# Kernel optimization log

Measured on AMD Instinct MI355X. Metric: run time of the kernel, lower is better.

The kernel has to match this reference:

```python
import jax, jax.numpy as jnp
import numpy as np

D_MODEL = 2048
SSM_RANK = 4            # ultimate_config.ar_ssm_max_rank
FFN_RANK = max(D_MODEL // 128, 2)  # = 16
EPS = 1e-6


def rmsnorm(x, w):
    # shared RMSNorm: x * w / rms(x)
    ms = jnp.mean(jnp.square(x), axis=-1, keepdims=True)
    return x * jax.lax.rsqrt(ms + EPS) * w


def ar_ssm(x, V, U, a_logit):
    # low-rank (rank r) semiseparable SSM:
    #   u_t = V^T x_t            [B,S,r]
    #   h_t = a * h_{t-1} + u_t  (per-rank learned decay a in (0,1))
    #   y_t = U h_t              [B,S,D]
    a = jax.nn.sigmoid(a_logit)               # [r]
    u = jnp.einsum('bsd,dr->bsr', x, V)       # [B,S,r]
    u_t = jnp.swapaxes(u, 0, 1)               # [S,B,r]

    def step(h, u_s):
        h = a * h + u_s
        return h, h

    h0 = jnp.zeros(u_t.shape[1:], dtype=x.dtype)   # [B,r]
    h_last, hs = jax.lax.scan(step, h0, u_t)        # hs: [S,B,r]
    hs = jnp.swapaxes(hs, 0, 1)                     # [B,S,r]
    y = jnp.einsum('bsr,dr->bsd', hs, U)
    return y, h_last


def ffn(x, W1, W2):
    return jnp.einsum('bsr,rd->bsd', jax.nn.gelu(jnp.einsum('bsd,dr->bsr', x, W1)), W2)


def setup_inputs() -> dict:
    key = jax.random.key(0)
    ks = jax.random.split(key, 7)
    B, S, D, R, RF = 4, 4096, D_MODEL, SSM_RANK, FFN_RANK
    x = jax.random.normal(ks[0], (B, S, D), dtype=jnp.float32)
    norm_w = jnp.ones((D,), dtype=jnp.float32)
    V = jax.random.normal(ks[1], (D, R), dtype=jnp.float32) / np.sqrt(D)
    U = jax.random.normal(ks[2], (D, R), dtype=jnp.float32) / np.sqrt(R)
    a_logit = jax.random.normal(ks[3], (R,), dtype=jnp.float32)
    W1 = jax.random.normal(ks[4], (D, RF), dtype=jnp.float32) / np.sqrt(D)
    W2 = jax.random.normal(ks[5], (RF, D), dtype=jnp.float32) / np.sqrt(RF)
    return {"x": x, "norm_w": norm_w, "V": V, "U": U, "a_logit": a_logit, "W1": W1, "W2": W2}


def reference(x, norm_w, V, U, a_logit, W1, W2):
    x_ar, _ = ar_ssm(rmsnorm(x, norm_w), V, U, a_logit)
    x = x + x_ar
    x = x + ffn(rmsnorm(x, norm_w), W1, W2)
    return x
```

## Files before the change

kernel.cpp:

```cpp
#include <hip/hip_runtime.h>
#include <math.h>
#include <stdint.h>

#define D 2048
#define S_LEN 4096
#define NB 4
#define NTOK (NB * S_LEN)

__device__ __forceinline__ float gelu_tanh(float v) {
    const float c = 0.7978845608028654f;
    float t = tanhf(c * (v + 0.044715f * v * v * v));
    return 0.5f * v * (1.0f + t);
}

__device__ __forceinline__ void gload_lds16(const float* g, float* l) {
    __builtin_amdgcn_global_load_lds(
        (const __attribute__((address_space(1))) void*)g,
        (__attribute__((address_space(3))) void*)(uintptr_t)(uint32_t)(uintptr_t)l,
        16, 0, 0);
}

__global__ __launch_bounds__(256) void k0_transpose(
        const float* __restrict__ W1, const float* __restrict__ V, const float* __restrict__ U,
        float* __restrict__ W1t, float* __restrict__ Vt, float* __restrict__ Ut)
{
    const int id = blockIdx.x * 256 + threadIdx.x;
    if (id < D * 16) {
        const int d = id >> 4, f = id & 15;
        W1t[f * D + d] = W1[id];
    } else if (id < D * 16 + D * 4) {
        const int i2 = id - D * 16;
        Vt[(i2 & 3) * D + (i2 >> 2)] = V[i2];
    } else {
        const int i2 = id - D * 16 - D * 4;
        Ut[(i2 & 3) * D + (i2 >> 2)] = U[i2];
    }
}

__global__ __launch_bounds__(256, 4) void k1_u_kernel(
        const float* __restrict__ x, const float* __restrict__ nw,
        const float* __restrict__ Vt, float* __restrict__ u)
{
    const int gwave = (blockIdx.x * 256 + threadIdx.x) >> 6;
    const int lane  = threadIdx.x & 63;
    const int t0 = gwave * 2;

    float ss[2] = {0.f, 0.f};
    float uv[2][4] = {};

    #pragma unroll
    for (int j = 0; j < 8; ++j) {
        const int d0 = j * 256 + lane * 4;
        const float4 nw4 = *reinterpret_cast<const float4*>(nw + d0);
        float4 z4[2];
        #pragma unroll
        for (int tk = 0; tk < 2; ++tk) {
            const float4 xv = *reinterpret_cast<const float4*>(x + (size_t)(t0 + tk) * D + d0);
            ss[tk] += xv.x*xv.x + xv.y*xv.y + xv.z*xv.z + xv.w*xv.w;
            z4[tk].x = xv.x*nw4.x; z4[tk].y = xv.y*nw4.y;
            z4[tk].z = xv.z*nw4.z; z4[tk].w = xv.w*nw4.w;
        }
        #pragma unroll
        for (int r = 0; r < 4; ++r) {
            const float4 vv = *reinterpret_cast<const float4*>(Vt + r * D + d0);
            #pragma unroll
            for (int tk = 0; tk < 2; ++tk)
                uv[tk][r] += z4[tk].x*vv.x + z4[tk].y*vv.y + z4[tk].z*vv.z + z4[tk].w*vv.w;
        }
    }
    #pragma unroll
    for (int m = 1; m < 64; m <<= 1) {
        #pragma unroll
        for (int tk = 0; tk < 2; ++tk) {
            ss[tk] += __shfl_xor(ss[tk], m);
            #pragma unroll
            for (int r = 0; r < 4; ++r) uv[tk][r] += __shfl_xor(uv[tk][r], m);
        }
    }
    if (lane < 8) {
        float ssv = ss[0], uvv = uv[0][0];
        #pragma unroll
        for (int tk = 0; tk < 2; ++tk)
            #pragma unroll
            for (int r = 0; r < 4; ++r)
                if (lane == tk * 4 + r) { ssv = ss[tk]; uvv = uv[tk][r]; }
        const float rstd = rsqrtf(ssv * (1.0f / 2048.0f) + 1e-6f);
        u[(size_t)t0 * 4 + lane] = rstd * uvv;
    }
}

__global__ __launch_bounds__(256) void k2_scan_kernel(
        const float* __restrict__ u, const float* __restrict__ a_logit,
        float* __restrict__ hs)
{
    __shared__ float lds[256];
    const int b = blockIdx.x >> 2;
    const int r = blockIdx.x & 3;
    const int i = threadIdx.x;
    const float a = 1.0f / (1.0f + expf(-a_logit[r]));
    const float* up = u  + (size_t)b * S_LEN * 4 + r;
    float*       hp = hs + (size_t)b * S_LEN * 4 + r;

    float ul[16];
    float h = 0.f;
    const int s0 = i * 16;
    #pragma unroll
    for (int k = 0; k < 16; ++k) { ul[k] = up[(size_t)(s0 + k) * 4]; h = a * h + ul[k]; }

    const float a2 = a*a, a4 = a2*a2, a8 = a4*a4;
    float m = a8 * a8;
    float run = h;
    lds[i] = run;
    for (int off = 1; off < 256; off <<= 1) {
        __syncthreads();
        const float v = (i >= off) ? lds[i - off] : 0.f;
        __syncthreads();
        run += m * v;
        lds[i] = run;
        m *= m;
    }
    __syncthreads();
    float hh = (i == 0) ? 0.f : lds[i - 1];
    #pragma unroll
    for (int k = 0; k < 16; ++k) { hh = a * hh + ul[k]; hp[(size_t)(s0 + k) * 4] = hh; }
}

#define SLICE_F 5376
__global__ __launch_bounds__(256) void k3_fused_kernel(
        const float* __restrict__ x, const float* __restrict__ nw,
        const float* __restrict__ Ut, const float* __restrict__ hs,
        const float* __restrict__ W1t, const float* __restrict__ W2,
        float* __restrict__ out)
{
    __shared__ float buf[2][SLICE_F];
    __shared__ float reds[4][2][20];
    __shared__ float tvs[4][32];
    const int w = threadIdx.x >> 6;
    const int lane = threadIdx.x & 63;
    const int t0 = (blockIdx.x * 4 + w) * 2;
    const float4* hs4 = reinterpret_cast<const float4*>(hs);
    float4 hv[2];
    #pragma unroll
    for (int tk = 0; tk < 2; ++tk) hv[tk] = hs4[t0 + tk];

    float ss[2] = {0.f, 0.f};
    float pf[2][16] = {};

    for (int s = w; s < 21; s += 4) {
        const float* src = (s == 0) ? (nw)
                         : (s < 5)  ? (Ut + (size_t)(s - 1) * D)
                                    : (W1t + (size_t)(s - 5) * D);
        gload_lds16(src + lane * 4, &buf[0][s * 256 + lane * 4]);
    }
    __syncthreads();

    for (int j = 0; j < 8; ++j) {
        const int cur = j & 1;
        if (j < 7) {
            const int jn = (j + 1) * 256;
            for (int s = w; s < 21; s += 4) {
                const float* src = (s == 0) ? (nw + jn)
                                 : (s < 5)  ? (Ut + (size_t)(s - 1) * D + jn)
                                            : (W1t + (size_t)(s - 5) * D + jn);
                gload_lds16(src + lane * 4, &buf[cur ^ 1][s * 256 + lane * 4]);
            }
        }
        const float* bw = buf[cur];
        const int d0 = j * 256 + lane * 4;
        const float4 nw4 = *reinterpret_cast<const float4*>(bw + lane * 4);
        float4 ut[4];
        #pragma unroll
        for (int r = 0; r < 4; ++r)
            ut[r] = *reinterpret_cast<const float4*>(bw + 256 + r * 256 + lane * 4);
        float4 z4[2];
        #pragma unroll
        for (int tk = 0; tk < 2; ++tk) {
            const float4 xv = *reinterpret_cast<const float4*>(x + (size_t)(t0 + tk) * D + d0);
            const float x20 = xv.x + hv[tk].x*ut[0].x + hv[tk].y*ut[1].x + hv[tk].z*ut[2].x + hv[tk].w*ut[3].x;
            const float x21 = xv.y + hv[tk].x*ut[0].y + hv[tk].y*ut[1].y + hv[tk].z*ut[2].y + hv[tk].w*ut[3].y;
            const float x22 = xv.z + hv[tk].x*ut[0].z + hv[tk].y*ut[1].z + hv[tk].z*ut[2].z + hv[tk].w*ut[3].z;
            const float x23 = xv.w + hv[tk].x*ut[0].w + hv[tk].y*ut[1].w + hv[tk].z*ut[2].w + hv[tk].w*ut[3].w;
            ss[tk] += x20*x20 + x21*x21 + x22*x22 + x23*x23;
            float4 x2v; x2v.x = x20; x2v.y = x21; x2v.z = x22; x2v.w = x23;
            *reinterpret_cast<float4*>(out + (size_t)(t0 + tk) * D + d0) = x2v;
            z4[tk].x = x20*nw4.x; z4[tk].y = x21*nw4.y;
            z4[tk].z = x22*nw4.z; z4[tk].w = x23*nw4.w;
        }
        #pragma unroll
        for (int f = 0; f < 16; ++f) {
            const float4 wv = *reinterpret_cast<const float4*>(bw + 1280 + f * 256 + lane * 4);
            #pragma unroll
            for (int tk = 0; tk < 2; ++tk)
                pf[tk][f] += z4[tk].x*wv.x + z4[tk].y*wv.y + z4[tk].z*wv.z + z4[tk].w*wv.w;
        }
        __syncthreads();
    }

    #pragma unroll
    for (int m = 1; m < 64; m <<= 1) {
        #pragma unroll
        for (int tk = 0; tk < 2; ++tk) {
            ss[tk] += __shfl_xor(ss[tk], m);
            #pragma unroll
            for (int f = 0; f < 16; ++f) pf[tk][f] += __shfl_xor(pf[tk][f], m);
        }
    }
    if (lane == 0) {
        #pragma unroll
        for (int tk = 0; tk < 2; ++tk) {
            reds[w][tk][16] = ss[tk];
            #pragma unroll
            for (int f = 0; f < 16; ++f) reds[w][tk][f] = pf[tk][f];
        }
    }
    __syncthreads();
    if (lane < 32) {
        const int mytk = lane >> 4, myf = lane & 15;
        const float rstd = rsqrtf(reds[w][mytk][16] * (1.0f / 2048.0f) + 1e-6f);
        tvs[w][lane] = gelu_tanh(rstd * reds[w][mytk][myf]);
    }
    __syncthreads();
    float tvv[2][16];
    #pragma unroll
    for (int tk = 0; tk < 2; ++tk)
        #pragma unroll
        for (int f = 0; f < 16; ++f) tvv[tk][f] = tvs[w][tk * 16 + f];

    for (int s = w; s < 16; s += 4)
        gload_lds16(W2 + (size_t)s * D + lane * 4, &buf[0][s * 256 + lane * 4]);
    __syncthreads();

    for (int j = 0; j < 8; ++j) {
        const int cur = j & 1;
        if (j < 7) {
            const int jn = (j + 1) * 256;
            for (int s = w; s < 16; s += 4)
                gload_lds16(W2 + (size_t)s * D + jn + lane * 4, &buf[cur ^ 1][s * 256 + lane * 4]);
        }
        const float* bw = buf[cur];
        const int d0 = j * 256 + lane * 4;
        float4 acc[2];
        #pragma unroll
        for (int tk = 0; tk < 2; ++tk)
            acc[tk] = *reinterpret_cast<const float4*>(out + (size_t)(t0 + tk) * D + d0);
        #pragma unroll
        for (int f = 0; f < 16; ++f) {
            const float4 w2v = *reinterpret_cast<const float4*>(bw + f * 256 + lane * 4);
            #pragma unroll
            for (int tk = 0; tk < 2; ++tk) {
                acc[tk].x += tvv[tk][f] * w2v.x;
                acc[tk].y += tvv[tk][f] * w2v.y;
                acc[tk].z += tvv[tk][f] * w2v.z;
                acc[tk].w += tvv[tk][f] * w2v.w;
            }
        }
        #pragma unroll
        for (int tk = 0; tk < 2; ++tk)
            *reinterpret_cast<float4*>(out + (size_t)(t0 + tk) * D + d0) = acc[tk];
        __syncthreads();
    }
}

extern "C" void kernel_launch(void* const* d_in, const int* in_sizes, int n_in,
                              void* d_out, int out_size, void* d_ws, size_t ws_size,
                              hipStream_t stream)
{
    (void)in_sizes; (void)n_in; (void)out_size; (void)ws_size;
    const float* x  = (const float*)d_in[0];
    const float* nw = (const float*)d_in[1];
    const float* V  = (const float*)d_in[2];
    const float* U  = (const float*)d_in[3];
    const float* al = (const float*)d_in[4];
    const float* W1 = (const float*)d_in[5];
    const float* W2 = (const float*)d_in[6];
    float* out = (float*)d_out;
    float* u   = (float*)d_ws;
    float* hs  = u + (size_t)NTOK * 4;
    float* W1t = hs + (size_t)NTOK * 4;
    float* Vt  = W1t + (size_t)16 * D;
    float* Ut  = Vt + (size_t)4 * D;

    k0_transpose  <<<dim3(192),       dim3(256), 0, stream>>>(W1, V, U, W1t, Vt, Ut);
    k1_u_kernel   <<<dim3(NTOK / 8),  dim3(256), 0, stream>>>(x, nw, Vt, u);
    k2_scan_kernel<<<dim3(16),        dim3(256), 0, stream>>>(u, al, hs);
    k3_fused_kernel<<<dim3(NTOK / 8), dim3(256), 0, stream>>>(x, nw, Ut, hs, W1t, W2, out);
}
```

Before: 339.0 us.

## Recompute residual in second pass, stage weights in LDS, vectorize scan over ranks

The fused kernel no longer writes the intermediate x+SSM residual to the output and reads it back. The second pass recomputes it from x, hs and U, with U staged in LDS next to W2, which removes one full-tensor write and read of output traffic. The u kernel now stages the norm weights and V in LDS once per block instead of reading them from global memory per wave. The scan uses one 1024-thread block per batch that handles all four ranks as float4, in place of 16 blocks each handling one rank with strided loads. This cuts scattered accesses, but the scan now runs on only four blocks.

```diff
diff --git a/kernel.cpp b/kernel.cpp
--- a/kernel.cpp
+++ b/kernel.cpp
@@ -37,13 +37,21 @@
     }
 }
 
-__global__ __launch_bounds__(256, 4) void k1_u_kernel(
+__global__ __launch_bounds__(256) void k1_u_kernel(
         const float* __restrict__ x, const float* __restrict__ nw,
         const float* __restrict__ Vt, float* __restrict__ u)
 {
-    const int gwave = (blockIdx.x * 256 + threadIdx.x) >> 6;
+    __shared__ float lw[10240];
+    const int w = threadIdx.x >> 6;
     const int lane  = threadIdx.x & 63;
-    const int t0 = gwave * 2;
+    const int t0 = ((blockIdx.x * 256 + threadIdx.x) >> 6) * 2;
+
+    for (int s = w; s < 40; s += 4) {
+        const int base = s * 256;
+        const float* src = (base < 2048) ? (nw + base) : (Vt + base - 2048);
+        gload_lds16(src + lane * 4, &lw[base + lane * 4]);
+    }
+    __syncthreads();
 
     float ss[2] = {0.f, 0.f};
     float uv[2][4] = {};
@@ -51,7 +59,7 @@
     #pragma unroll
     for (int j = 0; j < 8; ++j) {
         const int d0 = j * 256 + lane * 4;
-        const float4 nw4 = *reinterpret_cast<const float4*>(nw + d0);
+        const float4 nw4 = *reinterpret_cast<const float4*>(lw + d0);
         float4 z4[2];
         #pragma unroll
         for (int tk = 0; tk < 2; ++tk) {
@@ -62,7 +70,7 @@
         }
         #pragma unroll
         for (int r = 0; r < 4; ++r) {
-            const float4 vv = *reinterpret_cast<const float4*>(Vt + r * D + d0);
+            const float4 vv = *reinterpret_cast<const float4*>(lw + 2048 + r * 2048 + d0);
             #pragma unroll
             for (int tk = 0; tk < 2; ++tk)
                 uv[tk][r] += z4[tk].x*vv.x + z4[tk].y*vv.y + z4[tk].z*vv.z + z4[tk].w*vv.w;
@@ -89,40 +97,58 @@
     }
 }
 
-__global__ __launch_bounds__(256) void k2_scan_kernel(
+__global__ __launch_bounds__(1024) void k2_scan_kernel(
         const float* __restrict__ u, const float* __restrict__ a_logit,
         float* __restrict__ hs)
 {
-    __shared__ float lds[256];
-    const int b = blockIdx.x >> 2;
-    const int r = blockIdx.x & 3;
+    __shared__ float4 lds[1024];
+    const int b = blockIdx.x;
     const int i = threadIdx.x;
-    const float a = 1.0f / (1.0f + expf(-a_logit[r]));
-    const float* up = u  + (size_t)b * S_LEN * 4 + r;
-    float*       hp = hs + (size_t)b * S_LEN * 4 + r;
-
-    float ul[16];
-    float h = 0.f;
-    const int s0 = i * 16;
-    #pragma unroll
-    for (int k = 0; k < 16; ++k) { ul[k] = up[(size_t)(s0 + k) * 4]; h = a * h + ul[k]; }
-
-    const float a2 = a*a, a4 = a2*a2, a8 = a4*a4;
-    float m = a8 * a8;
-    float run = h;
+    const float4 al4 = *reinterpret_cast<const float4*>(a_logit);
+    float4 a;
+    a.x = 1.0f / (1.0f + expf(-al4.x));
+    a.y = 1.0f / (1.0f + expf(-al4.y));
+    a.z = 1.0f / (1.0f + expf(-al4.z));
+    a.w = 1.0f / (1.0f + expf(-al4.w));
+    const float4* up = reinterpret_cast<const float4*>(u) + (size_t)b * S_LEN;
+    float4*       hp = reinterpret_cast<float4*>(hs)      + (size_t)b * S_LEN;
+
+    const int s0 = i * 4;
+    float4 ul[4];
+    float4 h; h.x = 0.f; h.y = 0.f; h.z = 0.f; h.w = 0.f;
+    #pragma unroll
+    for (int k = 0; k < 4; ++k) {
+        ul[k] = up[s0 + k];
+        h.x = a.x * h.x + ul[k].x; h.y = a.y * h.y + ul[k].y;
+        h.z = a.z * h.z + ul[k].z; h.w = a.w * h.w + ul[k].w;
+    }
+
+    float4 m;
+    m.x = a.x*a.x; m.y = a.y*a.y; m.z = a.z*a.z; m.w = a.w*a.w;
+    m.x *= m.x; m.y *= m.y; m.z *= m.z; m.w *= m.w;
+    float4 run = h;
     lds[i] = run;
-    for (int off = 1; off < 256; off <<= 1) {
+    for (int off = 1; off < 1024; off <<= 1) {
         __syncthreads();
-        const float v = (i >= off) ? lds[i - off] : 0.f;
+        float4 v;
+        if (i >= off) v = lds[i - off];
+        else { v.x = 0.f; v.y = 0.f; v.z = 0.f; v.w = 0.f; }
         __syncthreads();
-        run += m * v;
+        run.x += m.x * v.x; run.y += m.y * v.y;
+        run.z += m.z * v.z; run.w += m.w * v.w;
         lds[i] = run;
-        m *= m;
-    }
-    __syncthreads();
-    float hh = (i == 0) ? 0.f : lds[i - 1];
-    #pragma unroll
-    for (int k = 0; k < 16; ++k) { hh = a * hh + ul[k]; hp[(size_t)(s0 + k) * 4] = hh; }
+        m.x *= m.x; m.y *= m.y; m.z *= m.z; m.w *= m.w;
+    }
+    __syncthreads();
+    float4 hh;
+    if (i == 0) { hh.x = 0.f; hh.y = 0.f; hh.z = 0.f; hh.w = 0.f; }
+    else hh = lds[i - 1];
+    #pragma unroll
+    for (int k = 0; k < 4; ++k) {
+        hh.x = a.x * hh.x + ul[k].x; hh.y = a.y * hh.y + ul[k].y;
+        hh.z = a.z * hh.z + ul[k].z; hh.w = a.w * hh.w + ul[k].w;
+        hp[s0 + k] = hh;
+    }
 }
 
 #define SLICE_F 5376
@@ -181,8 +207,6 @@
             const float x22 = xv.z + hv[tk].x*ut[0].z + hv[tk].y*ut[1].z + hv[tk].z*ut[2].z + hv[tk].w*ut[3].z;
             const float x23 = xv.w + hv[tk].x*ut[0].w + hv[tk].y*ut[1].w + hv[tk].z*ut[2].w + hv[tk].w*ut[3].w;
             ss[tk] += x20*x20 + x21*x21 + x22*x22 + x23*x23;
-            float4 x2v; x2v.x = x20; x2v.y = x21; x2v.z = x22; x2v.w = x23;
-            *reinterpret_cast<float4*>(out + (size_t)(t0 + tk) * D + d0) = x2v;
             z4[tk].x = x20*nw4.x; z4[tk].y = x21*nw4.y;
             z4[tk].z = x22*nw4.z; z4[tk].w = x23*nw4.w;
         }
@@ -226,26 +250,41 @@
         #pragma unroll
         for (int f = 0; f < 16; ++f) tvv[tk][f] = tvs[w][tk * 16 + f];
 
-    for (int s = w; s < 16; s += 4)
-        gload_lds16(W2 + (size_t)s * D + lane * 4, &buf[0][s * 256 + lane * 4]);
+    for (int s = w; s < 20; s += 4) {
+        const float* src = (s < 4) ? (Ut + (size_t)s * D)
+                                   : (W2 + (size_t)(s - 4) * D);
+        gload_lds16(src + lane * 4, &buf[0][s * 256 + lane * 4]);
+    }
     __syncthreads();
 
     for (int j = 0; j < 8; ++j) {
         const int cur = j & 1;
         if (j < 7) {
             const int jn = (j + 1) * 256;
-            for (int s = w; s < 16; s += 4)
-                gload_lds16(W2 + (size_t)s * D + jn + lane * 4, &buf[cur ^ 1][s * 256 + lane * 4]);
+            for (int s = w; s < 20; s += 4) {
+                const float* src = (s < 4) ? (Ut + (size_t)s * D + jn)
+                                           : (W2 + (size_t)(s - 4) * D + jn);
+                gload_lds16(src + lane * 4, &buf[cur ^ 1][s * 256 + lane * 4]);
+            }
         }
         const float* bw = buf[cur];
         const int d0 = j * 256 + lane * 4;
+        float4 ut[4];
+        #pragma unroll
+        for (int r = 0; r < 4; ++r)
+            ut[r] = *reinterpret_cast<const float4*>(bw + r * 256 + lane * 4);
         float4 acc[2];
         #pragma unroll
-        for (int tk = 0; tk < 2; ++tk)
-            acc[tk] = *reinterpret_cast<const float4*>(out + (size_t)(t0 + tk) * D + d0);
+        for (int tk = 0; tk < 2; ++tk) {
+            const float4 xv = *reinterpret_cast<const float4*>(x + (size_t)(t0 + tk) * D + d0);
+            acc[tk].x = xv.x + hv[tk].x*ut[0].x + hv[tk].y*ut[1].x + hv[tk].z*ut[2].x + hv[tk].w*ut[3].x;
+            acc[tk].y = xv.y + hv[tk].x*ut[0].y + hv[tk].y*ut[1].y + hv[tk].z*ut[2].y + hv[tk].w*ut[3].y;
+            acc[tk].z = xv.z + hv[tk].x*ut[0].z + hv[tk].y*ut[1].z + hv[tk].z*ut[2].z + hv[tk].w*ut[3].z;
+            acc[tk].w = xv.w + hv[tk].x*ut[0].w + hv[tk].y*ut[1].w + hv[tk].z*ut[2].w + hv[tk].w*ut[3].w;
+        }
         #pragma unroll
         for (int f = 0; f < 16; ++f) {
-            const float4 w2v = *reinterpret_cast<const float4*>(bw + f * 256 + lane * 4);
+            const float4 w2v = *reinterpret_cast<const float4*>(bw + 1024 + f * 256 + lane * 4);
             #pragma unroll
             for (int tk = 0; tk < 2; ++tk) {
                 acc[tk].x += tvv[tk][f] * w2v.x;
@@ -280,8 +319,8 @@
     float* Vt  = W1t + (size_t)16 * D;
     float* Ut  = Vt + (size_t)4 * D;
 
-    k0_transpose  <<<dim3(192),       dim3(256), 0, stream>>>(W1, V, U, W1t, Vt, Ut);
-    k1_u_kernel   <<<dim3(NTOK / 8),  dim3(256), 0, stream>>>(x, nw, Vt, u);
-    k2_scan_kernel<<<dim3(16),        dim3(256), 0, stream>>>(u, al, hs);
-    k3_fused_kernel<<<dim3(NTOK / 8), dim3(256), 0, stream>>>(x, nw, Ut, hs, W1t, W2, out);
-}
+    k0_transpose  <<<dim3(192),       dim3(256),  0, stream>>>(W1, V, U, W1t, Vt, Ut);
+    k1_u_kernel   <<<dim3(NTOK / 8),  dim3(256),  0, stream>>>(x, nw, Vt, u);
+    k2_scan_kernel<<<dim3(NB),        dim3(1024), 0, stream>>>(u, al, hs);
+    k3_fused_kernel<<<dim3(NTOK / 8), dim3(256),  0, stream>>>(x, nw, Ut, hs, W1t, W2, out);
+}
```

Result: faster. 320.7 us (-5.4%).
